# Kernel tuning notes

Measured on AMD Instinct MI355X. Metric: run time of the kernel, lower is better.

The kernel has to match this reference:

```python
import jax, jax.numpy as jnp
import numpy as np

N = 100000   # nodes
E = 600000   # edges
B = 512      # graphs in batch
H = 128      # hidden dim
ED = 8       # edge feature dim
TWO48 = float(2 ** 48 - 1)


def _w(k, shape, fan_in):
    return jax.random.normal(k, shape, jnp.float32) * (1.0 / np.sqrt(fan_in))


def setup_inputs() -> dict:
    key = jax.random.key(0)
    ks = jax.random.split(key, 32)
    inp = {}
    inp["s_node_ids"] = jax.random.randint(ks[0], (N,), 0, 2 ** 31 - 1, dtype=jnp.int32)
    inp["s_edge_index"] = jax.random.randint(ks[1], (2, E), 0, N, dtype=jnp.int32)
    inp["s_edge_attr"] = jax.random.normal(ks[2], (E, ED), jnp.float32)
    inp["s_batch"] = jnp.sort(jax.random.randint(ks[3], (N,), 0, B, dtype=jnp.int32))
    inp["depth"] = jax.random.uniform(ks[4], (B,), jnp.float32)
    # id_mlp: Linear(1,H) -> ReLU -> Linear(H,H)
    inp["id_w1"] = _w(ks[5], (1, H), 1); inp["id_b1"] = jnp.zeros((H,), jnp.float32)
    inp["id_w2"] = _w(ks[6], (H, H), H); inp["id_b2"] = jnp.zeros((H,), jnp.float32)
    # edge_mlp: Linear(ED,H) -> ReLU -> Linear(H,H)
    inp["ed_w1"] = _w(ks[7], (ED, H), ED); inp["ed_b1"] = jnp.zeros((H,), jnp.float32)
    inp["ed_w2"] = _w(ks[8], (H, H), H); inp["ed_b2"] = jnp.zeros((H,), jnp.float32)
    # GINEConv nn MLPs: Linear(H,H) -> ReLU -> Linear(H,H)
    inp["c1_w1"] = _w(ks[9], (H, H), H); inp["c1_b1"] = jnp.zeros((H,), jnp.float32)
    inp["c1_w2"] = _w(ks[10], (H, H), H); inp["c1_b2"] = jnp.zeros((H,), jnp.float32)
    inp["c2_w1"] = _w(ks[11], (H, H), H); inp["c2_b1"] = jnp.zeros((H,), jnp.float32)
    inp["c2_w2"] = _w(ks[12], (H, H), H); inp["c2_b2"] = jnp.zeros((H,), jnp.float32)
    inp["rg_w1"] = _w(ks[13], (H + 1, H), H + 1); inp["rg_b1"] = jnp.zeros((H,), jnp.float32)
    inp["rg_w2"] = _w(ks[14], (H, 1), H); inp["rg_b2"] = jnp.zeros((1,), jnp.float32)
    return inp


def _mlp2(x, w1, b1, w2, b2):
    return jax.nn.relu(x @ w1 + b1) @ w2 + b2


def _gine(x, src, dst, e, w1, b1, w2, b2):
    # message = ReLU(x_j + e), sum-aggregated at dst; out = nn((1+eps)*x + aggr), eps=0
    msg = jax.nn.relu(x[src] + e)                       # [E, H]
    aggr = jax.ops.segment_sum(msg, dst, num_segments=N)  # [N, H]
    return _mlp2(x + aggr, w1, b1, w2, b2)


def _global_mean(x, batch):
    sums = jax.ops.segment_sum(x, batch, num_segments=B)                          # [B, H]
    cnts = jax.ops.segment_sum(jnp.ones((x.shape[0], 1), x.dtype), batch, num_segments=B)
    return sums / jnp.maximum(cnts, 1.0)


def reference(s_node_ids, s_edge_index, s_edge_attr, s_batch, depth,
              id_w1, id_b1, id_w2, id_b2,
              ed_w1, ed_b1, ed_w2, ed_b2,
              c1_w1, c1_b1, c1_w2, c1_b2,
              c2_w1, c2_b1, c2_w2, c2_b2,
              rg_w1, rg_b1, rg_w2, rg_b2):
    src, dst = s_edge_index[0], s_edge_index[1]
    x0 = jnp.clip(s_node_ids.astype(jnp.float32) / TWO48, 0.0, 1.0)[:, None]  # [N,1]
    x = _mlp2(x0, id_w1, id_b1, id_w2, id_b2)                                 # [N,H]
    e = _mlp2(s_edge_attr, ed_w1, ed_b1, ed_w2, ed_b2)                        # [E,H]
    x = jax.nn.relu(_gine(x, src, dst, e, c1_w1, c1_b1, c1_w2, c1_b2))
    x = jax.nn.relu(_gine(x, src, dst, e, c2_w1, c2_b1, c2_w2, c2_b2))
    rep = jnp.concatenate([_global_mean(x, s_batch), depth[:, None]], axis=1)  # [B,H+1]
    return _mlp2(rep, rg_w1, rg_b1, rg_w2, rg_b2)[:, 0]                        # [B]
```

## Files before the change

kernel.cpp:

```cpp
#include <hip/hip_runtime.h>
#include <hip/hip_bf16.h>

#define N_NODES 100000
#define N_EDGES 600000
#define NB      512
#define H       128
#define ED      8
#define SCAN_CHUNK 1024
#define N_CHUNKS   98

typedef __attribute__((ext_vector_type(8))) short short8;
typedef __attribute__((ext_vector_type(4))) float f32x4;
typedef unsigned short u16;
typedef unsigned int   u32;

static __device__ __forceinline__ u16 f2bf(float f) {
    u32 u = __float_as_uint(f);
    u32 r = u + 0x7fffu + ((u >> 16) & 1u);
    return (u16)(r >> 16);
}
static __device__ __forceinline__ float bf2f(u32 h) {
    return __uint_as_float(h << 16);
}

__global__ __launch_bounds__(256) void pack_all_kernel(
    const float* __restrict__ W0, const float* __restrict__ W1,
    const float* __restrict__ W2, const float* __restrict__ W3,
    const float* __restrict__ W4, const float* __restrict__ W5,
    const float* __restrict__ W6,
    short8* __restrict__ O0, short8* __restrict__ O1,
    short8* __restrict__ O2, short8* __restrict__ O3,
    short8* __restrict__ O4, short8* __restrict__ O5,
    short8* __restrict__ O6)
{
    int gid = blockIdx.x * 256 + threadIdx.x;
    const int total = 512 + 6 * 2048;
    if (gid >= total) return;
    const float* W; short8* O; int Krows, kkmax, slot;
    if (gid < 512) { W = W0; O = O0; Krows = ED; kkmax = 1; slot = gid; }
    else {
        int m = (gid - 512) / 2048;
        slot = (gid - 512) % 2048;
        Krows = H; kkmax = 4;
        switch (m) {
            case 0: W = W1; O = O1; break;
            case 1: W = W2; O = O2; break;
            case 2: W = W3; O = O3; break;
            case 3: W = W4; O = O4; break;
            case 4: W = W5; O = O5; break;
            default: W = W6; O = O6; break;
        }
    }
    int lane = slot & 63;
    int t = slot >> 6;
    int nt = t & 1; t >>= 1;
    int kk = t % kkmax;
    int w  = t / kkmax;
    int quad = lane >> 4, n15 = lane & 15;
    int n = w * 32 + nt * 16 + n15;
    short8 v;
    #pragma unroll
    for (int j = 0; j < 8; j++) {
        int k = kk * 32 + quad * 8 + j;
        v[j] = (k < Krows) ? (short)f2bf(W[k * H + n]) : (short)0;
    }
    O[slot] = v;
}

__global__ __launch_bounds__(256) void hist_kernel(
    const int* __restrict__ edge_index, int* __restrict__ counts)
{
    int e = blockIdx.x * 256 + threadIdx.x;
    if (e < N_EDGES) atomicAdd(&counts[edge_index[N_EDGES + e]], 1);
}

__global__ __launch_bounds__(SCAN_CHUNK) void scan1_kernel(
    const int* __restrict__ counts, int* __restrict__ chunk_scan,
    int* __restrict__ bsum_raw)
{
    __shared__ int s[SCAN_CHUNK];
    int tid = threadIdx.x;
    int gid = blockIdx.x * SCAN_CHUNK + tid;
    int v = counts[gid];
    s[tid] = v;
    __syncthreads();
    #pragma unroll
    for (int off = 1; off < SCAN_CHUNK; off <<= 1) {
        int t = (tid >= off) ? s[tid - off] : 0;
        __syncthreads();
        s[tid] += t;
        __syncthreads();
    }
    chunk_scan[gid] = s[tid] - v;
    if (tid == SCAN_CHUNK - 1) bsum_raw[blockIdx.x] = s[tid];
}

__global__ __launch_bounds__(128) void scan2_kernel(
    const int* __restrict__ bsum_raw, int* __restrict__ bsum_scan)
{
    __shared__ int s[128];
    int tid = threadIdx.x;
    int v = (tid < N_CHUNKS) ? bsum_raw[tid] : 0;
    s[tid] = v;
    __syncthreads();
    #pragma unroll
    for (int off = 1; off < 128; off <<= 1) {
        int t = (tid >= off) ? s[tid - off] : 0;
        __syncthreads();
        s[tid] += t;
        __syncthreads();
    }
    bsum_scan[tid] = s[tid] - v;
}

__global__ __launch_bounds__(256) void fill_kernel(
    const int* __restrict__ edge_index,
    const int* __restrict__ chunk_scan, const int* __restrict__ bsum_scan,
    int* __restrict__ counts, int* __restrict__ src_list,
    int* __restrict__ pos_of)
{
    int e = blockIdx.x * 256 + threadIdx.x;
    if (e >= N_EDGES) return;
    int src = edge_index[e];
    int dst = edge_index[N_EDGES + e];
    int slot = atomicAdd(&counts[dst], -1) - 1;
    int pos = chunk_scan[dst] + bsum_scan[dst >> 10] + slot;
    src_list[pos] = src;
    pos_of[e] = pos;
}

__global__ __launch_bounds__(256) void node_mlp_mfma(
    const int* __restrict__ ids,
    const float* __restrict__ w1, const float* __restrict__ b1,
    const short8* __restrict__ pW2, const float* __restrict__ b2,
    u16* __restrict__ x_out)
{
    __shared__ u16 sH[64 * 136];
    __shared__ float s_x0[64];
    int tid = threadIdx.x;
    int w = tid >> 6, lane = tid & 63, quad = lane >> 4, n15 = lane & 15;
    short8 fW2[4][2];
    #pragma unroll
    for (int kk = 0; kk < 4; kk++) {
        fW2[kk][0] = pW2[((w * 4 + kk) * 2 + 0) * 64 + lane];
        fW2[kk][1] = pW2[((w * 4 + kk) * 2 + 1) * 64 + lane];
    }
    float rb2[2] = { b2[w * 32 + n15], b2[w * 32 + 16 + n15] };
    float w1c = w1[tid & 127], b1c = b1[tid & 127];
    const int ntile = (N_NODES + 63) / 64;
    for (int tile = blockIdx.x; tile < ntile; tile += gridDim.x) {
        int row0 = tile * 64;
        if (tid < 64) {
            int n = row0 + tid;
            float x0 = (n < N_NODES) ? (float)ids[n] / 281474976710655.0f : 0.0f;
            s_x0[tid] = fminf(fmaxf(x0, 0.0f), 1.0f);
        }
        __syncthreads();
        int half = tid >> 7, c = tid & 127;
        #pragma unroll 8
        for (int rr = 0; rr < 32; rr++) {
            int r = half + rr * 2;
            sH[r * 136 + c] = f2bf(fmaxf(s_x0[r] * w1c + b1c, 0.0f));
        }
        __syncthreads();
        f32x4 acc[4][2];
        #pragma unroll
        for (int s = 0; s < 4; s++) { acc[s][0] = (f32x4){0,0,0,0}; acc[s][1] = (f32x4){0,0,0,0}; }
        #pragma unroll
        for (int kk = 0; kk < 4; kk++) {
            #pragma unroll
            for (int s = 0; s < 4; s++) {
                short8 a = *(const short8*)&sH[(s * 16 + n15) * 136 + kk * 32 + quad * 8];
                acc[s][0] = __builtin_amdgcn_mfma_f32_16x16x32_bf16(a, fW2[kk][0], acc[s][0], 0, 0, 0);
                acc[s][1] = __builtin_amdgcn_mfma_f32_16x16x32_bf16(a, fW2[kk][1], acc[s][1], 0, 0, 0);
            }
        }
        #pragma unroll
        for (int s = 0; s < 4; s++)
            #pragma unroll
            for (int nt = 0; nt < 2; nt++) {
                int col = w * 32 + nt * 16 + n15;
                #pragma unroll
                for (int reg = 0; reg < 4; reg++) {
                    int n = row0 + s * 16 + quad * 4 + reg;
                    if (n < N_NODES)
                        x_out[(long)n * H + col] = f2bf(acc[s][nt][reg] + rb2[nt]);
                }
            }
        __syncthreads();
    }
}

__global__ __launch_bounds__(256) void edge_mlp_mfma(
    const float* __restrict__ attr,
    const int* __restrict__ pos_of,
    const short8* __restrict__ pW1, const float* __restrict__ b1,
    const short8* __restrict__ pW2, const float* __restrict__ b2,
    u16* __restrict__ e_perm)
{
    __shared__ u16 sA[64 * 40];
    __shared__ u16 sH[64 * 136];
    __shared__ int sPos[64];
    int tid = threadIdx.x;
    int w = tid >> 6, lane = tid & 63, quad = lane >> 4, n15 = lane & 15;
    short8 fW1[2];
    fW1[0] = pW1[(w * 2 + 0) * 64 + lane];
    fW1[1] = pW1[(w * 2 + 1) * 64 + lane];
    short8 fW2[4][2];
    #pragma unroll
    for (int kk = 0; kk < 4; kk++) {
        fW2[kk][0] = pW2[((w * 4 + kk) * 2 + 0) * 64 + lane];
        fW2[kk][1] = pW2[((w * 4 + kk) * 2 + 1) * 64 + lane];
    }
    float rb1[2] = { b1[w * 32 + n15], b1[w * 32 + 16 + n15] };
    float rb2[2] = { b2[w * 32 + n15], b2[w * 32 + 16 + n15] };
    const int ntile = N_EDGES / 64;
    for (int tile = blockIdx.x; tile < ntile; tile += gridDim.x) {
        int row0 = tile * 64;
        if (tid < 64) sPos[tid] = pos_of[row0 + tid];
        if (tid >= 64 && tid < 192) {
            int t2 = tid - 64;
            int r = t2 >> 1, c4 = (t2 & 1) * 4;
            float4 v = *(const float4*)&attr[(long)(row0 + r) * ED + c4];
            ushort4 o;
            o.x = f2bf(v.x); o.y = f2bf(v.y); o.z = f2bf(v.z); o.w = f2bf(v.w);
            *(ushort4*)&sA[r * 40 + c4] = o;
        } else if (tid >= 192) {
            int idx = tid - 192;
            for (; idx < 192; idx += 64) {
                int r = idx / 3, c8 = 8 + (idx % 3) * 8;
                *(uint4*)&sA[r * 40 + c8] = make_uint4(0, 0, 0, 0);
            }
        }
        __syncthreads();
        f32x4 acc[4][2];
        #pragma unroll
        for (int s = 0; s < 4; s++) { acc[s][0] = (f32x4){0,0,0,0}; acc[s][1] = (f32x4){0,0,0,0}; }
        #pragma unroll
        for (int s = 0; s < 4; s++) {
            short8 a = *(const short8*)&sA[(s * 16 + n15) * 40 + quad * 8];
            acc[s][0] = __builtin_amdgcn_mfma_f32_16x16x32_bf16(a, fW1[0], acc[s][0], 0, 0, 0);
            acc[s][1] = __builtin_amdgcn_mfma_f32_16x16x32_bf16(a, fW1[1], acc[s][1], 0, 0, 0);
        }
        #pragma unroll
        for (int s = 0; s < 4; s++)
            #pragma unroll
            for (int nt = 0; nt < 2; nt++) {
                int col = w * 32 + nt * 16 + n15;
                #pragma unroll
                for (int reg = 0; reg < 4; reg++)
                    sH[(s * 16 + quad * 4 + reg) * 136 + col] =
                        f2bf(fmaxf(acc[s][nt][reg] + rb1[nt], 0.0f));
            }
        __syncthreads();
        #pragma unroll
        for (int s = 0; s < 4; s++) { acc[s][0] = (f32x4){0,0,0,0}; acc[s][1] = (f32x4){0,0,0,0}; }
        #pragma unroll
        for (int kk = 0; kk < 4; kk++) {
            #pragma unroll
            for (int s = 0; s < 4; s++) {
                short8 a = *(const short8*)&sH[(s * 16 + n15) * 136 + kk * 32 + quad * 8];
                acc[s][0] = __builtin_amdgcn_mfma_f32_16x16x32_bf16(a, fW2[kk][0], acc[s][0], 0, 0, 0);
                acc[s][1] = __builtin_amdgcn_mfma_f32_16x16x32_bf16(a, fW2[kk][1], acc[s][1], 0, 0, 0);
            }
        }
        #pragma unroll
        for (int s = 0; s < 4; s++)
            #pragma unroll
            for (int nt = 0; nt < 2; nt++) {
                int col = w * 32 + nt * 16 + n15;
                #pragma unroll
                for (int reg = 0; reg < 4; reg++) {
                    long r = sPos[s * 16 + quad * 4 + reg];
                    e_perm[r * H + col] = f2bf(acc[s][nt][reg] + rb2[nt]);
                }
            }
        __syncthreads();
    }
}

__global__ __launch_bounds__(256) void aggregate_kernel(
    const int* __restrict__ src_list,
    const int* __restrict__ chunk_scan, const int* __restrict__ bsum_scan,
    const u16* __restrict__ e_perm,
    const u16* __restrict__ x,
    u16* __restrict__ xs_out)
{
    int wave = threadIdx.x >> 6;
    int lane = threadIdx.x & 63;
    int fo = lane * 2;
    const int ngroups = N_NODES / 4;
    for (int g = blockIdx.x; g < ngroups; g += gridDim.x) {
        int n = g * 4 + wave;
        int beg = chunk_scan[n]     + bsum_scan[n >> 10];
        int end = chunk_scan[n + 1] + bsum_scan[(n + 1) >> 10];
        float a0 = 0.0f, a1 = 0.0f;
        for (int j0 = beg; j0 < end; j0 += 64) {
            int m = min(64, end - j0);
            int sv = (lane < m) ? src_list[j0 + lane] : 0;
            for (int j = 0; j < m; j++) {
                int src = __shfl(sv, j);
                u32 xv = *(const u32*)&x[(long)src * H + fo];
                u32 ev = *(const u32*)&e_perm[(long)(j0 + j) * H + fo];
                a0 += fmaxf(bf2f(xv & 0xffff) + bf2f(ev & 0xffff), 0.0f);
                a1 += fmaxf(bf2f(xv >> 16)    + bf2f(ev >> 16),    0.0f);
            }
        }
        u32 xself = *(const u32*)&x[(long)n * H + fo];
        float o0 = bf2f(xself & 0xffff) + a0;
        float o1 = bf2f(xself >> 16)    + a1;
        *(u32*)&xs_out[(long)n * H + fo] = (u32)f2bf(o0) | ((u32)f2bf(o1) << 16);
    }
}

__global__ __launch_bounds__(256) void conv_mlp_mfma(
    const u16* __restrict__ xs,
    const short8* __restrict__ pW1, const float* __restrict__ b1,
    const short8* __restrict__ pW2, const float* __restrict__ b2,
    u16* __restrict__ x_out)
{
    __shared__ u16 sA[64 * 136];
    __shared__ u16 sH[64 * 136];
    int tid = threadIdx.x;
    int w = tid >> 6, lane = tid & 63, quad = lane >> 4, n15 = lane & 15;
    short8 fW1[4][2], fW2[4][2];
    #pragma unroll
    for (int kk = 0; kk < 4; kk++) {
        fW1[kk][0] = pW1[((w * 4 + kk) * 2 + 0) * 64 + lane];
        fW1[kk][1] = pW1[((w * 4 + kk) * 2 + 1) * 64 + lane];
        fW2[kk][0] = pW2[((w * 4 + kk) * 2 + 0) * 64 + lane];
        fW2[kk][1] = pW2[((w * 4 + kk) * 2 + 1) * 64 + lane];
    }
    float rb1[2] = { b1[w * 32 + n15], b1[w * 32 + 16 + n15] };
    float rb2[2] = { b2[w * 32 + n15], b2[w * 32 + 16 + n15] };
    const int ntile = (N_NODES + 63) / 64;
    for (int tile = blockIdx.x; tile < ntile; tile += gridDim.x) {
        int row0 = tile * 64;
        for (int idx = tid; idx < 64 * 16; idx += 256) {
            int r = idx >> 4, c8 = (idx & 15) << 3;
            int n = row0 + r;
            uint4 v = make_uint4(0, 0, 0, 0);
            if (n < N_NODES) v = *(const uint4*)&xs[(long)n * H + c8];
            *(uint4*)&sA[r * 136 + c8] = v;
        }
        __syncthreads();
        f32x4 acc[4][2];
        #pragma unroll
        for (int s = 0; s < 4; s++) { acc[s][0] = (f32x4){0,0,0,0}; acc[s][1] = (f32x4){0,0,0,0}; }
        #pragma unroll
        for (int kk = 0; kk < 4; kk++) {
            #pragma unroll
            for (int s = 0; s < 4; s++) {
                short8 a = *(const short8*)&sA[(s * 16 + n15) * 136 + kk * 32 + quad * 8];
                acc[s][0] = __builtin_amdgcn_mfma_f32_16x16x32_bf16(a, fW1[kk][0], acc[s][0], 0, 0, 0);
                acc[s][1] = __builtin_amdgcn_mfma_f32_16x16x32_bf16(a, fW1[kk][1], acc[s][1], 0, 0, 0);
            }
        }
        #pragma unroll
        for (int s = 0; s < 4; s++)
            #pragma unroll
            for (int nt = 0; nt < 2; nt++) {
                int col = w * 32 + nt * 16 + n15;
                #pragma unroll
                for (int reg = 0; reg < 4; reg++)
                    sH[(s * 16 + quad * 4 + reg) * 136 + col] =
                        f2bf(fmaxf(acc[s][nt][reg] + rb1[nt], 0.0f));
            }
        __syncthreads();
        #pragma unroll
        for (int s = 0; s < 4; s++) { acc[s][0] = (f32x4){0,0,0,0}; acc[s][1] = (f32x4){0,0,0,0}; }
        #pragma unroll
        for (int kk = 0; kk < 4; kk++) {
            #pragma unroll
            for (int s = 0; s < 4; s++) {
                short8 a = *(const short8*)&sH[(s * 16 + n15) * 136 + kk * 32 + quad * 8];
                acc[s][0] = __builtin_amdgcn_mfma_f32_16x16x32_bf16(a, fW2[kk][0], acc[s][0], 0, 0, 0);
                acc[s][1] = __builtin_amdgcn_mfma_f32_16x16x32_bf16(a, fW2[kk][1], acc[s][1], 0, 0, 0);
            }
        }
        #pragma unroll
        for (int s = 0; s < 4; s++)
            #pragma unroll
            for (int nt = 0; nt < 2; nt++) {
                int col = w * 32 + nt * 16 + n15;
                #pragma unroll
                for (int reg = 0; reg < 4; reg++) {
                    int n = row0 + s * 16 + quad * 4 + reg;
                    if (n < N_NODES)
                        x_out[(long)n * H + col] = f2bf(fmaxf(acc[s][nt][reg] + rb2[nt], 0.0f));
                }
            }
        __syncthreads();
    }
}

__global__ __launch_bounds__(256) void pool_kernel(
    const u16* __restrict__ x, const int* __restrict__ batch,
    float* __restrict__ sums, float* __restrict__ cnt)
{
    int sg   = threadIdx.x >> 6;
    int lane = threadIdx.x & 63;
    int fo = lane * 2;
    const int nper = (N_NODES + gridDim.x - 1) / gridDim.x;
    int n0 = blockIdx.x * nper;
    int n1 = min(n0 + nper, N_NODES);
    int cur = -1;
    float a0 = 0.0f, a1 = 0.0f, c = 0.0f;
    for (int n = n0 + sg; n < n1; n += 4) {
        int b = batch[n];
        if (b != cur) {
            if (cur >= 0) {
                atomicAdd(&sums[cur * H + fo],     a0);
                atomicAdd(&sums[cur * H + fo + 1], a1);
                if (lane == 0) atomicAdd(&cnt[cur], c);
            }
            a0 = a1 = 0.0f; c = 0.0f; cur = b;
        }
        u32 xv = *(const u32*)&x[(long)n * H + fo];
        a0 += bf2f(xv & 0xffff);
        a1 += bf2f(xv >> 16);
        c += 1.0f;
    }
    if (cur >= 0) {
        atomicAdd(&sums[cur * H + fo],     a0);
        atomicAdd(&sums[cur * H + fo + 1], a1);
        if (lane == 0) atomicAdd(&cnt[cur], c);
    }
}

__global__ __launch_bounds__(128) void regressor_kernel(
    const float* __restrict__ sums, const float* __restrict__ cnt,
    const float* __restrict__ depth,
    const float* __restrict__ w1, const float* __restrict__ b1,
    const float* __restrict__ w2, const float* __restrict__ b2,
    float* __restrict__ out)
{
    __shared__ float s_mean[H];
    __shared__ float s_red[2];
    int b = blockIdx.x;
    int j = threadIdx.x;
    float c = fmaxf(cnt[b], 1.0f);
    s_mean[j] = sums[b * H + j] / c;
    __syncthreads();
    float h = b1[j];
    #pragma unroll 8
    for (int k = 0; k < H; k++) h += s_mean[k] * w1[k * H + j];
    h += depth[b] * w1[H * H + j];
    h = fmaxf(h, 0.0f);
    float p = h * w2[j];
    #pragma unroll
    for (int off = 32; off >= 1; off >>= 1) p += __shfl_down(p, off, 64);
    if ((j & 63) == 0) s_red[j >> 6] = p;
    __syncthreads();
    if (j == 0) out[b] = s_red[0] + s_red[1] + b2[0];
}

extern "C" void kernel_launch(void* const* d_in, const int* in_sizes, int n_in,
                              void* d_out, int out_size, void* d_ws, size_t ws_size,
                              hipStream_t stream)
{
    const int*   ids   = (const int*)  d_in[0];
    const int*   eidx  = (const int*)  d_in[1];
    const float* eattr = (const float*)d_in[2];
    const int*   batch = (const int*)  d_in[3];
    const float* depth = (const float*)d_in[4];
    const float* id_w1 = (const float*)d_in[5];
    const float* id_b1 = (const float*)d_in[6];
    const float* id_w2 = (const float*)d_in[7];
    const float* id_b2 = (const float*)d_in[8];
    const float* ed_w1 = (const float*)d_in[9];
    const float* ed_b1 = (const float*)d_in[10];
    const float* ed_w2 = (const float*)d_in[11];
    const float* ed_b2 = (const float*)d_in[12];
    const float* c1_w1 = (const float*)d_in[13];
    const float* c1_b1 = (const float*)d_in[14];
    const float* c1_w2 = (const float*)d_in[15];
    const float* c1_b2 = (const float*)d_in[16];
    const float* c2_w1 = (const float*)d_in[17];
    const float* c2_b1 = (const float*)d_in[18];
    const float* c2_w2 = (const float*)d_in[19];
    const float* c2_b2 = (const float*)d_in[20];
    const float* rg_w1 = (const float*)d_in[21];
    const float* rg_b1 = (const float*)d_in[22];
    const float* rg_w2 = (const float*)d_in[23];
    const float* rg_b2 = (const float*)d_in[24];

    char* ws = (char*)d_ws;
    u16*   e_buf    = (u16*)  (ws);
    u16*   x_buf    = (u16*)  (ws + 153600000);
    u16*   xs_buf   = (u16*)  (ws + 179200000);
    float* sums_buf = (float*)(ws + 204800000);
    float* cnt_buf  = (float*)(ws + 205062144);
    int*   counts   = (int*)  (ws + 205064192);
    int*   chunk_sc = (int*)  (ws + 205465600);
    int*   bsum_raw = (int*)  (ws + 205867008);
    int*   bsum_sc  = (int*)  (ws + 205867520);
    int*   src_list = (int*)  (ws + 205868032);
    int*   pos_of   = (int*)  (ws + 208268032);
    short8* ed_w1p  = (short8*)(ws + 210668032);
    short8* ed_w2p  = (short8*)(ws + 210676224);
    short8* c1_w1p  = (short8*)(ws + 210708992);
    short8* c1_w2p  = (short8*)(ws + 210741760);
    short8* c2_w1p  = (short8*)(ws + 210774528);
    short8* c2_w2p  = (short8*)(ws + 210807296);
    short8* id_w2p  = (short8*)(ws + 210840064);

    pack_all_kernel<<<50, 256, 0, stream>>>(
        ed_w1, ed_w2, c1_w1, c1_w2, c2_w1, c2_w2, id_w2,
        ed_w1p, ed_w2p, c1_w1p, c1_w2p, c2_w1p, c2_w2p, id_w2p);

    hipMemsetAsync(counts, 0, 401408, stream);
    hist_kernel <<<(N_EDGES + 255) / 256, 256, 0, stream>>>(eidx, counts);
    scan1_kernel<<<N_CHUNKS, SCAN_CHUNK, 0, stream>>>(counts, chunk_sc, bsum_raw);
    scan2_kernel<<<1, 128, 0, stream>>>(bsum_raw, bsum_sc);
    fill_kernel <<<(N_EDGES + 255) / 256, 256, 0, stream>>>(eidx, chunk_sc, bsum_sc,
                                                            counts, src_list, pos_of);

    node_mlp_mfma<<<768, 256, 0, stream>>>(ids, id_w1, id_b1, id_w2p, id_b2, x_buf);
    edge_mlp_mfma<<<2048, 256, 0, stream>>>(eattr, pos_of, ed_w1p, ed_b1, ed_w2p, ed_b2, e_buf);

    aggregate_kernel<<<8192, 256, 0, stream>>>(src_list, chunk_sc, bsum_sc, e_buf, x_buf, xs_buf);
    conv_mlp_mfma<<<1563, 256, 0, stream>>>(xs_buf, c1_w1p, c1_b1, c1_w2p, c1_b2, x_buf);

    aggregate_kernel<<<8192, 256, 0, stream>>>(src_list, chunk_sc, bsum_sc, e_buf, x_buf, xs_buf);
    conv_mlp_mfma<<<1563, 256, 0, stream>>>(xs_buf, c2_w1p, c2_b1, c2_w2p, c2_b2, x_buf);

    hipMemsetAsync(sums_buf, 0, (size_t)(NB * H + NB) * 4, stream);
    pool_kernel<<<2048, 256, 0, stream>>>(x_buf, batch, sums_buf, cnt_buf);
    regressor_kernel<<<NB, 128, 0, stream>>>(sums_buf, cnt_buf, depth,
                                             rg_w1, rg_b1, rg_w2, rg_b2, (float*)d_out);
}
```

Measured before the change: 438.1 us.

## Vectorize aggregation gathers, stage MLP outputs for coalesced stores, add row_ptr

The aggregate kernel now has each wave process two edges per step, with each lane loading 8-byte chunks, and combines the two halves with a cross-lane shuffle. The edge and conv MLP kernels now stage results in shared memory and write full 16-byte rows, replacing scattered 2-byte stores. Their input tiles are read straight from global memory into MFMA fragments, dropping the shared-memory staging and one barrier. A precomputed row_ptr array replaces the two-array offset lookup. Costs are an extra small kernel launch and extra barriers, plus wasted lanes when a node has an odd number of edges.

```diff
diff --git a/kernel.cpp b/kernel.cpp
--- a/kernel.cpp
+++ b/kernel.cpp
@@ -113,6 +113,14 @@
     bsum_scan[tid] = s[tid] - v;
 }
 
+__global__ __launch_bounds__(256) void rowptr_kernel(
+    const int* __restrict__ chunk_scan, const int* __restrict__ bsum_scan,
+    int* __restrict__ row_ptr)
+{
+    int gid = blockIdx.x * 256 + threadIdx.x;
+    if (gid <= N_NODES) row_ptr[gid] = chunk_scan[gid] + bsum_scan[gid >> 10];
+}
+
 __global__ __launch_bounds__(256) void fill_kernel(
     const int* __restrict__ edge_index,
     const int* __restrict__ chunk_scan, const int* __restrict__ bsum_scan,
@@ -198,7 +206,6 @@
     const short8* __restrict__ pW2, const float* __restrict__ b2,
     u16* __restrict__ e_perm)
 {
-    __shared__ u16 sA[64 * 40];
     __shared__ u16 sH[64 * 136];
     __shared__ int sPos[64];
     int tid = threadIdx.x;
@@ -217,31 +224,26 @@
     const int ntile = N_EDGES / 64;
     for (int tile = blockIdx.x; tile < ntile; tile += gridDim.x) {
         int row0 = tile * 64;
-        if (tid < 64) sPos[tid] = pos_of[row0 + tid];
-        if (tid >= 64 && tid < 192) {
-            int t2 = tid - 64;
-            int r = t2 >> 1, c4 = (t2 & 1) * 4;
-            float4 v = *(const float4*)&attr[(long)(row0 + r) * ED + c4];
-            ushort4 o;
-            o.x = f2bf(v.x); o.y = f2bf(v.y); o.z = f2bf(v.z); o.w = f2bf(v.w);
-            *(ushort4*)&sA[r * 40 + c4] = o;
-        } else if (tid >= 192) {
-            int idx = tid - 192;
-            for (; idx < 192; idx += 64) {
-                int r = idx / 3, c8 = 8 + (idx % 3) * 8;
-                *(uint4*)&sA[r * 40 + c8] = make_uint4(0, 0, 0, 0);
-            }
-        }
-        __syncthreads();
         f32x4 acc[4][2];
         #pragma unroll
         for (int s = 0; s < 4; s++) { acc[s][0] = (f32x4){0,0,0,0}; acc[s][1] = (f32x4){0,0,0,0}; }
         #pragma unroll
         for (int s = 0; s < 4; s++) {
-            short8 a = *(const short8*)&sA[(s * 16 + n15) * 40 + quad * 8];
+            short8 a = {0,0,0,0,0,0,0,0};
+            if (quad == 0) {
+                long r = row0 + s * 16 + n15;
+                float4 v0 = *(const float4*)&attr[r * ED];
+                float4 v1 = *(const float4*)&attr[r * ED + 4];
+                a[0] = (short)f2bf(v0.x); a[1] = (short)f2bf(v0.y);
+                a[2] = (short)f2bf(v0.z); a[3] = (short)f2bf(v0.w);
+                a[4] = (short)f2bf(v1.x); a[5] = (short)f2bf(v1.y);
+                a[6] = (short)f2bf(v1.z); a[7] = (short)f2bf(v1.w);
+            }
             acc[s][0] = __builtin_amdgcn_mfma_f32_16x16x32_bf16(a, fW1[0], acc[s][0], 0, 0, 0);
             acc[s][1] = __builtin_amdgcn_mfma_f32_16x16x32_bf16(a, fW1[1], acc[s][1], 0, 0, 0);
         }
+        __syncthreads();
+        if (tid < 64) sPos[tid] = pos_of[row0 + tid];
         #pragma unroll
         for (int s = 0; s < 4; s++)
             #pragma unroll
@@ -264,52 +266,77 @@
                 acc[s][1] = __builtin_amdgcn_mfma_f32_16x16x32_bf16(a, fW2[kk][1], acc[s][1], 0, 0, 0);
             }
         }
+        __syncthreads();
         #pragma unroll
         for (int s = 0; s < 4; s++)
             #pragma unroll
             for (int nt = 0; nt < 2; nt++) {
                 int col = w * 32 + nt * 16 + n15;
                 #pragma unroll
-                for (int reg = 0; reg < 4; reg++) {
-                    long r = sPos[s * 16 + quad * 4 + reg];
-                    e_perm[r * H + col] = f2bf(acc[s][nt][reg] + rb2[nt]);
-                }
-            }
-        __syncthreads();
+                for (int reg = 0; reg < 4; reg++)
+                    sH[(s * 16 + quad * 4 + reg) * 136 + col] =
+                        f2bf(acc[s][nt][reg] + rb2[nt]);
+            }
+        __syncthreads();
+        #pragma unroll
+        for (int it = 0; it < 4; it++) {
+            int rr = w * 4 + it * 16 + (lane >> 4);
+            long pos = sPos[rr];
+            uint4 v = *(const uint4*)&sH[rr * 136 + (lane & 15) * 8];
+            *(uint4*)&e_perm[pos * H + (lane & 15) * 8] = v;
+        }
     }
 }
 
 __global__ __launch_bounds__(256) void aggregate_kernel(
     const int* __restrict__ src_list,
-    const int* __restrict__ chunk_scan, const int* __restrict__ bsum_scan,
+    const int* __restrict__ row_ptr,
     const u16* __restrict__ e_perm,
     const u16* __restrict__ x,
     u16* __restrict__ xs_out)
 {
     int wave = threadIdx.x >> 6;
     int lane = threadIdx.x & 63;
-    int fo = lane * 2;
+    int half = lane >> 5;
+    int fo   = (lane & 31) * 4;
     const int ngroups = N_NODES / 4;
     for (int g = blockIdx.x; g < ngroups; g += gridDim.x) {
         int n = g * 4 + wave;
-        int beg = chunk_scan[n]     + bsum_scan[n >> 10];
-        int end = chunk_scan[n + 1] + bsum_scan[(n + 1) >> 10];
-        float a0 = 0.0f, a1 = 0.0f;
+        int beg = row_ptr[n];
+        int end = row_ptr[n + 1];
+        float a0 = 0.0f, a1 = 0.0f, a2 = 0.0f, a3 = 0.0f;
         for (int j0 = beg; j0 < end; j0 += 64) {
             int m = min(64, end - j0);
             int sv = (lane < m) ? src_list[j0 + lane] : 0;
-            for (int j = 0; j < m; j++) {
-                int src = __shfl(sv, j);
-                u32 xv = *(const u32*)&x[(long)src * H + fo];
-                u32 ev = *(const u32*)&e_perm[(long)(j0 + j) * H + fo];
-                a0 += fmaxf(bf2f(xv & 0xffff) + bf2f(ev & 0xffff), 0.0f);
-                a1 += fmaxf(bf2f(xv >> 16)    + bf2f(ev >> 16),    0.0f);
-            }
-        }
-        u32 xself = *(const u32*)&x[(long)n * H + fo];
-        float o0 = bf2f(xself & 0xffff) + a0;
-        float o1 = bf2f(xself >> 16)    + a1;
-        *(u32*)&xs_out[(long)n * H + fo] = (u32)f2bf(o0) | ((u32)f2bf(o1) << 16);
+            for (int k = 0; 2 * k < m; k++) {
+                int idx = 2 * k + half;
+                bool valid = idx < m;
+                int src = __shfl(sv, idx);
+                long p = j0 + (valid ? idx : 0);
+                uint2 ev = *(const uint2*)&e_perm[p * H + fo];
+                uint2 xv = *(const uint2*)&x[(long)src * H + fo];
+                float m0 = fmaxf(bf2f(xv.x & 0xffff) + bf2f(ev.x & 0xffff), 0.0f);
+                float m1 = fmaxf(bf2f(xv.x >> 16)    + bf2f(ev.x >> 16),    0.0f);
+                float m2 = fmaxf(bf2f(xv.y & 0xffff) + bf2f(ev.y & 0xffff), 0.0f);
+                float m3 = fmaxf(bf2f(xv.y >> 16)    + bf2f(ev.y >> 16),    0.0f);
+                if (valid) { a0 += m0; a1 += m1; a2 += m2; a3 += m3; }
+            }
+        }
+        a0 += __shfl_xor(a0, 32);
+        a1 += __shfl_xor(a1, 32);
+        a2 += __shfl_xor(a2, 32);
+        a3 += __shfl_xor(a3, 32);
+        uint2 xself = *(const uint2*)&x[(long)n * H + fo];
+        float o0 = bf2f(xself.x & 0xffff) + a0;
+        float o1 = bf2f(xself.x >> 16)    + a1;
+        float o2 = bf2f(xself.y & 0xffff) + a2;
+        float o3 = bf2f(xself.y >> 16)    + a3;
+        if (half == 0) {
+            uint2 o;
+            o.x = (u32)f2bf(o0) | ((u32)f2bf(o1) << 16);
+            o.y = (u32)f2bf(o2) | ((u32)f2bf(o3) << 16);
+            *(uint2*)&xs_out[(long)n * H + fo] = o;
+        }
     }
 }
 
@@ -319,7 +346,6 @@
     const short8* __restrict__ pW2, const float* __restrict__ b2,
     u16* __restrict__ x_out)
 {
-    __shared__ u16 sA[64 * 136];
     __shared__ u16 sH[64 * 136];
     int tid = threadIdx.x;
     int w = tid >> 6, lane = tid & 63, quad = lane >> 4, n15 = lane & 15;
@@ -336,14 +362,6 @@
     const int ntile = (N_NODES + 63) / 64;
     for (int tile = blockIdx.x; tile < ntile; tile += gridDim.x) {
         int row0 = tile * 64;
-        for (int idx = tid; idx < 64 * 16; idx += 256) {
-            int r = idx >> 4, c8 = (idx & 15) << 3;
-            int n = row0 + r;
-            uint4 v = make_uint4(0, 0, 0, 0);
-            if (n < N_NODES) v = *(const uint4*)&xs[(long)n * H + c8];
-            *(uint4*)&sA[r * 136 + c8] = v;
-        }
-        __syncthreads();
         f32x4 acc[4][2];
         #pragma unroll
         for (int s = 0; s < 4; s++) { acc[s][0] = (f32x4){0,0,0,0}; acc[s][1] = (f32x4){0,0,0,0}; }
@@ -351,11 +369,14 @@
         for (int kk = 0; kk < 4; kk++) {
             #pragma unroll
             for (int s = 0; s < 4; s++) {
-                short8 a = *(const short8*)&sA[(s * 16 + n15) * 136 + kk * 32 + quad * 8];
+                int r = row0 + s * 16 + n15;
+                short8 a = {0,0,0,0,0,0,0,0};
+                if (r < N_NODES) a = *(const short8*)&xs[(long)r * H + kk * 32 + quad * 8];
                 acc[s][0] = __builtin_amdgcn_mfma_f32_16x16x32_bf16(a, fW1[kk][0], acc[s][0], 0, 0, 0);
                 acc[s][1] = __builtin_amdgcn_mfma_f32_16x16x32_bf16(a, fW1[kk][1], acc[s][1], 0, 0, 0);
             }
         }
+        __syncthreads();
         #pragma unroll
         for (int s = 0; s < 4; s++)
             #pragma unroll
@@ -378,19 +399,26 @@
                 acc[s][1] = __builtin_amdgcn_mfma_f32_16x16x32_bf16(a, fW2[kk][1], acc[s][1], 0, 0, 0);
             }
         }
+        __syncthreads();
         #pragma unroll
         for (int s = 0; s < 4; s++)
             #pragma unroll
             for (int nt = 0; nt < 2; nt++) {
                 int col = w * 32 + nt * 16 + n15;
                 #pragma unroll
-                for (int reg = 0; reg < 4; reg++) {
-                    int n = row0 + s * 16 + quad * 4 + reg;
-                    if (n < N_NODES)
-                        x_out[(long)n * H + col] = f2bf(fmaxf(acc[s][nt][reg] + rb2[nt], 0.0f));
-                }
-            }
-        __syncthreads();
+                for (int reg = 0; reg < 4; reg++)
+                    sH[(s * 16 + quad * 4 + reg) * 136 + col] =
+                        f2bf(fmaxf(acc[s][nt][reg] + rb2[nt], 0.0f));
+            }
+        __syncthreads();
+        for (int i = tid; i < 64 * 16; i += 256) {
+            int rr = i >> 4, c8 = (i & 15) * 8;
+            int n = row0 + rr;
+            if (n < N_NODES) {
+                uint4 v = *(const uint4*)&sH[rr * 136 + c8];
+                *(uint4*)&x_out[(long)n * H + c8] = v;
+            }
+        }
     }
 }
 
@@ -504,6 +532,7 @@
     short8* c2_w1p  = (short8*)(ws + 210774528);
     short8* c2_w2p  = (short8*)(ws + 210807296);
     short8* id_w2p  = (short8*)(ws + 210840064);
+    int*   row_ptr  = (int*)  (ws + 210872832);
 
     pack_all_kernel<<<50, 256, 0, stream>>>(
         ed_w1, ed_w2, c1_w1, c1_w2, c2_w1, c2_w2, id_w2,
@@ -513,16 +542,17 @@
     hist_kernel <<<(N_EDGES + 255) / 256, 256, 0, stream>>>(eidx, counts);
     scan1_kernel<<<N_CHUNKS, SCAN_CHUNK, 0, stream>>>(counts, chunk_sc, bsum_raw);
     scan2_kernel<<<1, 128, 0, stream>>>(bsum_raw, bsum_sc);
+    rowptr_kernel<<<(N_NODES + 256) / 256, 256, 0, stream>>>(chunk_sc, bsum_sc, row_ptr);
     fill_kernel <<<(N_EDGES + 255) / 256, 256, 0, stream>>>(eidx, chunk_sc, bsum_sc,
                                                             counts, src_list, pos_of);
 
     node_mlp_mfma<<<768, 256, 0, stream>>>(ids, id_w1, id_b1, id_w2p, id_b2, x_buf);
     edge_mlp_mfma<<<2048, 256, 0, stream>>>(eattr, pos_of, ed_w1p, ed_b1, ed_w2p, ed_b2, e_buf);
 
-    aggregate_kernel<<<8192, 256, 0, stream>>>(src_list, chunk_sc, bsum_sc, e_buf, x_buf, xs_buf);
+    aggregate_kernel<<<8192, 256, 0, stream>>>(src_list, row_ptr, e_buf, x_buf, xs_buf);
     conv_mlp_mfma<<<1563, 256, 0, stream>>>(xs_buf, c1_w1p, c1_b1, c1_w2p, c1_b2, x_buf);
 
-    aggregate_kernel<<<8192, 256, 0, stream>>>(src_list, chunk_sc, bsum_sc, e_buf, x_buf, xs_buf);
+    aggregate_kernel<<<8192, 256, 0, stream>>>(src_list, row_ptr, e_buf, x_buf, xs_buf);
     conv_mlp_mfma<<<1563, 256, 0, stream>>>(xs_buf, c2_w1p, c2_b1, c2_w2p, c2_b2, x_buf);
 
     hipMemsetAsync(sums_buf, 0, (size_t)(NB * H + NB) * 4, stream);
```

Result: slower. 468.6 us (+7.0%).
